# Performance work log

Measured on AMD Instinct MI355X. Metric: run time of the kernel, lower is better.

Reference implementation:

```python
import jax, jax.numpy as jnp
import numpy as np

TOP_K = 2
NUM_EXPERTS = 64
AUX_COEF = 0.01


def setup_inputs() -> dict:
    key = jax.random.key(0)
    kx, kw = jax.random.split(key)
    B, S, D, E = 4, 4096, 2048, NUM_EXPERTS
    x = jax.random.normal(kx, (B, S, D), dtype=jnp.float32)
    # nn.Linear default init ~ U(-1/sqrt(D), 1/sqrt(D))
    W = jax.random.uniform(kw, (E, D), dtype=jnp.float32,
                           minval=-1.0 / np.sqrt(D), maxval=1.0 / np.sqrt(D))
    return {"x": x, "W": W}


def reference(x, W):
    B, S, D = x.shape
    E = W.shape[0]
    # router projection (no bias)
    logits = jnp.einsum('bsd,ed->bse', x, W)          # [B,S,E]
    probs = jax.nn.softmax(logits, axis=-1)           # [B,S,E]
    top_k_gates, top_k_indices = jax.lax.top_k(probs, TOP_K)  # [B,S,K]
    top_k_gates = top_k_gates / (jnp.sum(top_k_gates, axis=-1, keepdims=True) + 1e-9)
    # aux loss: fraction of routed slots per expert (one-hot mean) x mean router prob
    total_slots = B * S * TOP_K
    counts = jnp.zeros((E,), dtype=jnp.float32).at[top_k_indices.reshape(-1)].add(1.0)
    avg_tokens_per_expert = counts / total_slots      # == one_hot(idx).mean(dims 0,1,2)
    avg_router_prob = jnp.mean(probs, axis=(0, 1))    # [E]
    aux_loss = AUX_COEF * E * jnp.sum(avg_tokens_per_expert * avg_router_prob)
    return top_k_indices, top_k_gates, aux_loss
```

## Files before the change

### kernel.cpp

```cpp
#include <hip/hip_runtime.h>
#include <math.h>

#define NTOK 16384
#define DDIM 2048
#define NEXP 64
#define TM   16
#define NBLK (NTOK / TM)
#define NCH  32
#define NS   64

typedef _Float16 half4v __attribute__((ext_vector_type(4)));
typedef _Float16 half8v __attribute__((ext_vector_type(8)));
typedef float    f32x4  __attribute__((ext_vector_type(4)));

#define MFMA16(a, b, c) __builtin_amdgcn_mfma_f32_16x16x32_f16((a), (b), (c), 0, 0, 0)

__global__ __launch_bounds__(256) void prep_kernel(const float* __restrict__ W,
                                                   _Float16* __restrict__ Wh,
                                                   _Float16* __restrict__ Wl,
                                                   float* __restrict__ accg) {
    int idx = blockIdx.x * 256 + threadIdx.x;
    int e = idx >> 11, k = idx & 2047;
    float w = W[idx];
    _Float16 h = (_Float16)w;
    _Float16 l = (_Float16)(w - (float)h);
    int S = k >> 5, nb = e >> 4, nl = e & 15, q = (k >> 3) & 3, j = k & 7;
    size_t off = (size_t)S * 2048 + nb * 512 + q * 128 + nl * 8 + j;
    Wh[off] = h;
    Wl[off] = l;
    if (blockIdx.x == 0 && threadIdx.x < 128) accg[threadIdx.x] = 0.0f;
}

__device__ inline void cvt_store(_Float16* __restrict__ Hp, _Float16* __restrict__ Lp,
                                 int off, float4 v) {
    half4v h, l;
    h.x = (_Float16)v.x; l.x = (_Float16)(v.x - (float)h.x);
    h.y = (_Float16)v.y; l.y = (_Float16)(v.y - (float)h.y);
    h.z = (_Float16)v.z; l.z = (_Float16)(v.z - (float)h.z);
    h.w = (_Float16)v.w; l.w = (_Float16)(v.w - (float)h.w);
    *(half4v*)&Hp[off] = h;
    *(half4v*)&Lp[off] = l;
}

__global__ __launch_bounds__(256) void router_kernel(
    const float* __restrict__ x, const _Float16* __restrict__ Wh,
    const _Float16* __restrict__ Wl, float* __restrict__ accg,
    float* __restrict__ out)
{
    __shared__ __align__(16) _Float16 Ah[2][1024];
    __shared__ __align__(16) _Float16 Al[2][1024];
    __shared__ float lgt[TM][NEXP + 1];
    __shared__ float cnt[NEXP];

    const int tid  = threadIdx.x;
    const int lane = tid & 63;
    const int wv   = __builtin_amdgcn_readfirstlane(tid >> 6);
    const int m0   = blockIdx.x * TM;

    if (tid < NEXP) cnt[tid] = 0.0f;

    const int tok0 = tid >> 4;
    const int kk0  = (tid & 15) * 4;
    const int s0   = kk0 >> 5, q0 = (kk0 >> 3) & 3, j00 = kk0 & 7;
    const int offA = (s0 * 64 + q0 * 16 + tok0) * 8 + j00;

    const float* gx = x + (size_t)(m0 + tok0) * DDIM + kk0;

    const _Float16* whp = Wh + wv * 512 + lane * 8;
    const _Float16* wlp = Wl + wv * 512 + lane * 8;

    f32x4 acc = {0.f, 0.f, 0.f, 0.f};

    float4 stg[2];
    stg[0] = *(const float4*)(gx);
    stg[1] = *(const float4*)(gx + 64);
    half8v wbh[2], wbl[2];
    #pragma unroll
    for (int s = 0; s < 2; ++s) {
        wbh[s] = *(const half8v*)(whp + (size_t)s * 2048);
        wbl[s] = *(const half8v*)(wlp + (size_t)s * 2048);
    }

    for (int ch = 0; ch < NCH; ++ch) {
        const int p = ch & 1;
        cvt_store(&Ah[p][0], &Al[p][0], offA, stg[p]);
        const int cf = (ch + 2 < NCH) ? ch + 2 : 0;
        stg[p] = *(const float4*)(gx + cf * 64);
        __syncthreads();
        #pragma unroll
        for (int s = 0; s < 2; ++s) {
            const int Sg  = ch * 2 + s;
            const int SgN = (Sg + 2) & (NS - 1);
            half8v ah = *(const half8v*)&Ah[p][(s * 64 + lane) * 8];
            half8v al = *(const half8v*)&Al[p][(s * 64 + lane) * 8];
            half8v bh = wbh[s], bl = wbl[s];
            wbh[s] = *(const half8v*)(whp + (size_t)SgN * 2048);
            wbl[s] = *(const half8v*)(wlp + (size_t)SgN * 2048);
            acc = MFMA16(al, bh, acc);
            acc = MFMA16(ah, bl, acc);
            acc = MFMA16(ah, bh, acc);
        }
    }

    {
        const int q  = lane >> 4;
        const int nl = lane & 15;
        #pragma unroll
        for (int r = 0; r < 4; ++r)
            lgt[q * 4 + r][wv * 16 + nl] = acc[r];
    }
    __syncthreads();

    if (tid < 128) {
        const int m = tid >> 3;
        const int j = tid & 7;
        float l[8];
        #pragma unroll
        for (int i = 0; i < 8; ++i) l[i] = lgt[m][j * 8 + i];

        float mx = l[0];
        #pragma unroll
        for (int i = 1; i < 8; ++i) mx = fmaxf(mx, l[i]);
        #pragma unroll
        for (int off = 1; off < 8; off <<= 1) mx = fmaxf(mx, __shfl_xor(mx, off, 8));

        float ev[8];
        float zs = 0.f;
        float v1 = -INFINITY, v2 = -INFINITY;
        int i1 = 0, i2 = 0;
        #pragma unroll
        for (int i = 0; i < 8; ++i) {
            ev[i] = __expf(l[i] - mx);
            zs += ev[i];
            int e = j * 8 + i;
            if (l[i] > v1)      { v2 = v1; i2 = i1; v1 = l[i]; i1 = e; }
            else if (l[i] > v2) { v2 = l[i]; i2 = e; }
        }
        #pragma unroll
        for (int off = 1; off < 8; off <<= 1) zs += __shfl_xor(zs, off, 8);

        #pragma unroll
        for (int off = 1; off < 8; off <<= 1) {
            float ov1 = __shfl_xor(v1, off, 8);
            int   oi1 = __shfl_xor(i1, off, 8);
            float ov2 = __shfl_xor(v2, off, 8);
            int   oi2 = __shfl_xor(i2, off, 8);
            bool afirst = (v1 > ov1) || (v1 == ov1 && i1 < oi1);
            if (afirst) {
                bool t = (v2 > ov1) || (v2 == ov1 && i2 < oi1);
                v2 = t ? v2 : ov1;
                i2 = t ? i2 : oi1;
            } else {
                bool t = (ov2 > v1) || (ov2 == v1 && oi2 < i1);
                v2 = t ? ov2 : v1;
                i2 = t ? oi2 : i1;
                v1 = ov1;
                i1 = oi1;
            }
        }

        const float invz = 1.0f / zs;
        if (j == 0) {
            float p1 = invz;
            float p2 = __expf(v2 - mx) * invz;
            float sden = p1 + p2 + 1e-9f;
            int tok = m0 + m;
            out[tok * 2 + 0] = (float)i1;
            out[tok * 2 + 1] = (float)i2;
            out[32768 + tok * 2 + 0] = p1 / sden;
            out[32768 + tok * 2 + 1] = p2 / sden;
            atomicAdd(&cnt[i1], 1.0f);
            atomicAdd(&cnt[i2], 1.0f);
        }

        #pragma unroll
        for (int i = 0; i < 8; ++i) lgt[m][j * 8 + i] = ev[i] * invz;
    }
    __syncthreads();

    if (tid < NEXP) {
        atomicAdd(&accg[tid], cnt[tid]);
    } else if (tid < 128) {
        int e = tid - 64;
        float s = 0.f;
        #pragma unroll
        for (int t = 0; t < TM; ++t) s += lgt[t][e];
        atomicAdd(&accg[64 + e], s);
    }
}

__global__ void finalize_kernel(const float* __restrict__ accg,
                                float* __restrict__ out)
{
    int t = threadIdx.x;
    float c = accg[t];
    float p = accg[64 + t];
    float term = (c / (float)(NTOK * 2)) * (p / (float)NTOK);
    #pragma unroll
    for (int off = 1; off < 64; off <<= 1) term += __shfl_xor(term, off, 64);
    if (t == 0) out[65536] = 0.01f * (float)NEXP * term;
}

extern "C" void kernel_launch(void* const* d_in, const int* in_sizes, int n_in,
                              void* d_out, int out_size, void* d_ws, size_t ws_size,
                              hipStream_t stream) {
    const float* x = (const float*)d_in[0];
    const float* W = (const float*)d_in[1];
    float* out  = (float*)d_out;
    float* accg = (float*)d_ws;
    _Float16* Wh = (_Float16*)(accg + 128);
    _Float16* Wl = Wh + (size_t)DDIM * NEXP;

    prep_kernel<<<512, 256, 0, stream>>>(W, Wh, Wl, accg);
    router_kernel<<<NBLK, 256, 0, stream>>>(x, Wh, Wl, accg, out);
    finalize_kernel<<<1, 64, 0, stream>>>(accg, out);
}
```

Before: 215.6 us.

## Split K across waves with per-wave LDS staging and cross-wave logit reduction

```diff
diff --git a/kernel.cpp b/kernel.cpp
--- a/kernel.cpp
+++ b/kernel.cpp
@@ -6,8 +6,8 @@
 #define NEXP 64
 #define TM   16
 #define NBLK (NTOK / TM)
-#define NCH  32
-#define NS   64
+#define KPW  512
+#define NCHW 8
 
 typedef _Float16 half4v __attribute__((ext_vector_type(4)));
 typedef _Float16 half8v __attribute__((ext_vector_type(8)));
@@ -42,14 +42,14 @@
     *(half4v*)&Lp[off] = l;
 }
 
-__global__ __launch_bounds__(256) void router_kernel(
+__global__ __launch_bounds__(256, 4) void router_kernel(
     const float* __restrict__ x, const _Float16* __restrict__ Wh,
     const _Float16* __restrict__ Wl, float* __restrict__ accg,
     float* __restrict__ out)
 {
-    __shared__ __align__(16) _Float16 Ah[2][1024];
-    __shared__ __align__(16) _Float16 Al[2][1024];
-    __shared__ float lgt[TM][NEXP + 1];
+    __shared__ __align__(16) _Float16 Ah[4][1024];
+    __shared__ __align__(16) _Float16 Al[4][1024];
+    __shared__ float red[4][TM][NEXP + 1];
     __shared__ float cnt[NEXP];
 
     const int tid  = threadIdx.x;
@@ -59,46 +59,59 @@
 
     if (tid < NEXP) cnt[tid] = 0.0f;
 
-    const int tok0 = tid >> 4;
-    const int kk0  = (tid & 15) * 4;
-    const int s0   = kk0 >> 5, q0 = (kk0 >> 3) & 3, j00 = kk0 & 7;
-    const int offA = (s0 * 64 + q0 * 16 + tok0) * 8 + j00;
-
-    const float* gx = x + (size_t)(m0 + tok0) * DDIM + kk0;
-
-    const _Float16* whp = Wh + wv * 512 + lane * 8;
-    const _Float16* wlp = Wl + wv * 512 + lane * 8;
-
-    f32x4 acc = {0.f, 0.f, 0.f, 0.f};
-
-    float4 stg[2];
-    stg[0] = *(const float4*)(gx);
-    stg[1] = *(const float4*)(gx + 64);
-    half8v wbh[2], wbl[2];
+    _Float16* ah_buf = Ah[wv];
+    _Float16* al_buf = Al[wv];
+
+    const int tokb = lane >> 4;
+    const int kk   = (lane & 15) * 4;
+    const int S0   = kk >> 5, q0 = (kk >> 3) & 3, j0 = kk & 7;
+    const int offA = (S0 * 64 + q0 * 16 + tokb) * 8 + j0;
+
+    const int kb = wv * KPW;
+    const float* gx = x + (size_t)(m0 + tokb) * DDIM + kb + kk;
+
+    const _Float16* whp = Wh + lane * 8;
+    const _Float16* wlp = Wl + lane * 8;
+
+    f32x4 acc[4];
     #pragma unroll
-    for (int s = 0; s < 2; ++s) {
-        wbh[s] = *(const half8v*)(whp + (size_t)s * 2048);
-        wbl[s] = *(const half8v*)(wlp + (size_t)s * 2048);
-    }
-
-    for (int ch = 0; ch < NCH; ++ch) {
-        const int p = ch & 1;
-        cvt_store(&Ah[p][0], &Al[p][0], offA, stg[p]);
-        const int cf = (ch + 2 < NCH) ? ch + 2 : 0;
-        stg[p] = *(const float4*)(gx + cf * 64);
-        __syncthreads();
+    for (int nb = 0; nb < 4; ++nb) acc[nb] = (f32x4){0.f, 0.f, 0.f, 0.f};
+
+    float4 stg[2][4];
+    #pragma unroll
+    for (int c = 0; c < 2; ++c)
+        #pragma unroll
+        for (int i = 0; i < 4; ++i)
+            stg[c][i] = *(const float4*)(gx + (size_t)(4 * i) * DDIM + c * 64);
+
+    for (int c = 0; c < NCHW; ++c) {
+        const int p = c & 1;
+        #pragma unroll
+        for (int i = 0; i < 4; ++i)
+            cvt_store(ah_buf, al_buf, offA + 32 * i, stg[p][i]);
+        const int cf = (c + 2 < NCHW) ? c + 2 : 0;
+        #pragma unroll
+        for (int i = 0; i < 4; ++i)
+            stg[p][i] = *(const float4*)(gx + (size_t)(4 * i) * DDIM + cf * 64);
         #pragma unroll
         for (int s = 0; s < 2; ++s) {
-            const int Sg  = ch * 2 + s;
-            const int SgN = (Sg + 2) & (NS - 1);
-            half8v ah = *(const half8v*)&Ah[p][(s * 64 + lane) * 8];
-            half8v al = *(const half8v*)&Al[p][(s * 64 + lane) * 8];
-            half8v bh = wbh[s], bl = wbl[s];
-            wbh[s] = *(const half8v*)(whp + (size_t)SgN * 2048);
-            wbl[s] = *(const half8v*)(wlp + (size_t)SgN * 2048);
-            acc = MFMA16(al, bh, acc);
-            acc = MFMA16(ah, bl, acc);
-            acc = MFMA16(ah, bh, acc);
+            const int Sg = wv * 16 + c * 2 + s;
+            const _Float16* wh_s = whp + (size_t)Sg * 2048;
+            const _Float16* wl_s = wlp + (size_t)Sg * 2048;
+            half8v bh[4], bl[4];
+            #pragma unroll
+            for (int nb = 0; nb < 4; ++nb) {
+                bh[nb] = *(const half8v*)(wh_s + nb * 512);
+                bl[nb] = *(const half8v*)(wl_s + nb * 512);
+            }
+            half8v ah = *(const half8v*)&ah_buf[(s * 64 + lane) * 8];
+            half8v al = *(const half8v*)&al_buf[(s * 64 + lane) * 8];
+            #pragma unroll
+            for (int nb = 0; nb < 4; ++nb) {
+                acc[nb] = MFMA16(al, bh[nb], acc[nb]);
+                acc[nb] = MFMA16(ah, bl[nb], acc[nb]);
+                acc[nb] = MFMA16(ah, bh[nb], acc[nb]);
+            }
         }
     }
 
@@ -106,8 +119,10 @@
         const int q  = lane >> 4;
         const int nl = lane & 15;
         #pragma unroll
-        for (int r = 0; r < 4; ++r)
-            lgt[q * 4 + r][wv * 16 + nl] = acc[r];
+        for (int nb = 0; nb < 4; ++nb)
+            #pragma unroll
+            for (int r = 0; r < 4; ++r)
+                red[wv][q * 4 + r][nb * 16 + nl] = acc[nb][r];
     }
     __syncthreads();
 
@@ -116,7 +131,9 @@
         const int j = tid & 7;
         float l[8];
         #pragma unroll
-        for (int i = 0; i < 8; ++i) l[i] = lgt[m][j * 8 + i];
+        for (int i = 0; i < 8; ++i)
+            l[i] = (red[0][m][j * 8 + i] + red[1][m][j * 8 + i]) +
+                   (red[2][m][j * 8 + i] + red[3][m][j * 8 + i]);
 
         float mx = l[0];
         #pragma unroll
@@ -174,7 +191,7 @@
         }
 
         #pragma unroll
-        for (int i = 0; i < 8; ++i) lgt[m][j * 8 + i] = ev[i] * invz;
+        for (int i = 0; i < 8; ++i) red[0][m][j * 8 + i] = ev[i] * invz;
     }
     __syncthreads();
 
@@ -184,7 +201,7 @@
         int e = tid - 64;
         float s = 0.f;
         #pragma unroll
-        for (int t = 0; t < TM; ++t) s += lgt[t][e];
+        for (int t = 0; t < TM; ++t) s += red[0][t][e];
         atomicAdd(&accg[64 + e], s);
     }
 }
```

Result: slower. 220.6 us (+2.3%).
